# Performance work log

Measured on AMD Instinct MI355X. Metric: run time of the kernel, lower is better.

Reference implementation:

```python
import jax, jax.numpy as jnp
import numpy as np

DIM = 1024
NUM_HEADS = 16
HEAD_DIM = DIM // NUM_HEADS
SCALE = HEAD_DIM ** -0.5


def setup_inputs() -> dict:
    key = jax.random.key(0)
    ks = jax.random.split(key, 6)
    B, N, C = 2, 2048, DIM
    std = C ** -0.5
    return {
        "x_t": jax.random.normal(ks[0], (B, N, C), dtype=jnp.float32),
        "x_s": jax.random.normal(ks[1], (B, N, C), dtype=jnp.float32),
        "W_q": jax.random.normal(ks[2], (C, C), dtype=jnp.float32) * std,
        "W_kv": jax.random.normal(ks[3], (C, 2 * C), dtype=jnp.float32) * std,
        "W_fuse": jax.random.normal(ks[4], (C, C), dtype=jnp.float32) * std,
        "b_fuse": jax.random.normal(ks[5], (C,), dtype=jnp.float32) * 0.01,
    }


def reference(x_t, x_s, W_q, W_kv, W_fuse, b_fuse):
    B, N, C = x_t.shape
    H, D = NUM_HEADS, HEAD_DIM
    # q projection (no bias, qkv_bias=False): [B,N,C] -> [B,H,N,D]
    q = (x_t @ W_q).reshape(B, N, H, D).transpose(0, 2, 1, 3)
    # kv projection: [B,N,2C] -> k,v each [B,H,N,D]
    kv = (x_s @ W_kv).reshape(B, N, 2, H, D).transpose(2, 0, 3, 1, 4)
    k, v = kv[0], kv[1]
    # attention scores [B,H,N,N]
    attn = jnp.einsum("bhnd,bhmd->bhnm", q, k) * SCALE
    attn = jax.nn.softmax(attn, axis=-1)
    # weighted values -> [B,N,C]
    a = jnp.einsum("bhnm,bhmd->bhnd", attn, v).transpose(0, 2, 1, 3).reshape(B, N, C)
    # fuse projection (with bias); dropouts are identity (p=0)
    return a @ W_fuse + b_fuse
```

## Files before the change

### kernel.cpp

```cpp
#include <hip/hip_runtime.h>

#define SEQ 2048

typedef short short8 __attribute__((ext_vector_type(8)));
typedef float floatx4 __attribute__((ext_vector_type(4)));
typedef unsigned int uint2v __attribute__((ext_vector_type(2)));
typedef unsigned int uint4v __attribute__((ext_vector_type(4)));
typedef __fp16 f16x8 __attribute__((ext_vector_type(8)));

static __device__ __forceinline__ unsigned short f2bf(float f) {
    unsigned int u = __builtin_bit_cast(unsigned int, f);
    u = (u + 0x7fffu + ((u >> 16) & 1u)) >> 16;
    return (unsigned short)u;
}

#if __has_builtin(__builtin_amdgcn_cvt_pk_bf16_f32)
typedef __bf16 bf16x2 __attribute__((ext_vector_type(2)));
static __device__ __forceinline__ unsigned int pk_bf16(float a, float b) {
    bf16x2 v = __builtin_amdgcn_cvt_pk_bf16_f32(a, b);
    return __builtin_bit_cast(unsigned int, v);
}
#else
static __device__ __forceinline__ unsigned int pk_bf16(float a, float b) {
    return (unsigned int)f2bf(a) | ((unsigned int)f2bf(b) << 16);
}
#endif

static __device__ __forceinline__ unsigned int pk_f16(float a, float b) {
    auto v = __builtin_amdgcn_cvt_pkrtz(a, b);
    return __builtin_bit_cast(unsigned int, v);
}

#define GLD16(gp, lp)                                                        \
    __builtin_amdgcn_global_load_lds(                                        \
        (const __attribute__((address_space(1))) unsigned int*)(gp),         \
        (__attribute__((address_space(3))) unsigned int*)(lp), 16, 0, 0)

__global__ void cvt2_kernel(const float4* __restrict__ a, const float4* __restrict__ b,
                            ushort4* __restrict__ oa, ushort4* __restrict__ ob, float sa) {
    int i = blockIdx.x * blockDim.x + threadIdx.x;
    if (i < 1048576) {
        float4 v = a[i];
        ushort4 o;
        o.x = f2bf(v.x * sa); o.y = f2bf(v.y * sa);
        o.z = f2bf(v.z * sa); o.w = f2bf(v.w * sa);
        oa[i] = o;
    } else {
        int j = i - 1048576;
        float4 v = b[j];
        ushort4 o;
        o.x = f2bf(v.x); o.y = f2bf(v.y);
        o.z = f2bf(v.z); o.w = f2bf(v.w);
        ob[j] = o;
    }
}

__global__ void transpose_all(const float* __restrict__ Wq, const float* __restrict__ Wkv,
                              const float* __restrict__ Wf,
                              unsigned short* __restrict__ oq, unsigned short* __restrict__ okv,
                              unsigned short* __restrict__ of_) {
    __shared__ float tile[32][33];
    int bx = blockIdx.x;
    const float* in; unsigned short* out; int N, t;
    if (bx < 1024)      { in = Wq;  out = oq;  N = 1024; t = bx; }
    else if (bx < 3072) { in = Wkv; out = okv; N = 2048; t = bx - 1024; }
    else                { in = Wf;  out = of_; N = 1024; t = bx - 3072; }
    int nb = N >> 5;
    int n0 = (t % nb) * 32, k0 = (t / nb) * 32;
    int tx = threadIdx.x, ty = threadIdx.y;
#pragma unroll
    for (int i = 0; i < 4; i++)
        tile[ty + i * 8][tx] = in[(size_t)(k0 + ty + i * 8) * N + n0 + tx];
    __syncthreads();
#pragma unroll
    for (int i = 0; i < 4; i++)
        out[(size_t)(n0 + ty + i * 8) * 1024 + k0 + tx] = f2bf(tile[tx][ty + i * 8]);
}

__global__ __launch_bounds__(256, 3)
void gemm_qkv(const unsigned short* __restrict__ xt,
              const unsigned short* __restrict__ xs,
              const unsigned short* __restrict__ wq,
              const unsigned short* __restrict__ wkv,
              unsigned short* __restrict__ q_ws,
              unsigned short* __restrict__ k_ws,
              unsigned short* __restrict__ vt_ws) {
    __shared__ unsigned short sA[128][64];
    __shared__ unsigned short sB[128][64];
    int tid = threadIdx.x, wave = tid >> 6, lane = tid & 63;
    int l15 = lane & 15, quad = lane >> 4;
    int cx = blockIdx.x;
    bool isq = cx < 8;
    const unsigned short* A  = isq ? xt : xs;
    const unsigned short* Bt = isq ? wq : wkv;
    int C0 = (isq ? cx : cx - 8) * 128;
    int R0 = blockIdx.y * 128;
    int wr = (wave >> 1) * 64, wc = (wave & 1) * 64;
    int srow = lane >> 3, scol = (lane & 7) * 8;

    floatx4 acc[4][4];
#pragma unroll
    for (int i = 0; i < 4; i++)
#pragma unroll
        for (int j = 0; j < 4; j++) acc[i][j] = (floatx4){0.f, 0.f, 0.f, 0.f};

    for (int kt = 0; kt < 16; kt++) {
        __syncthreads();
#pragma unroll
        for (int c = 0; c < 4; c++) {
            int rb = wave * 32 + c * 8;
            GLD16(&A [(size_t)(R0 + rb + srow) * 1024 + kt * 64 + scol], &sA[rb][0]);
            GLD16(&Bt[(size_t)(C0 + rb + srow) * 1024 + kt * 64 + scol], &sB[rb][0]);
        }
        __syncthreads();
#pragma unroll
        for (int ks = 0; ks < 2; ks++) {
            short8 af[4], bf[4];
#pragma unroll
            for (int mt = 0; mt < 4; mt++)
                af[mt] = *(const short8*)&sA[wr + mt * 16 + l15][ks * 32 + quad * 8];
#pragma unroll
            for (int nt = 0; nt < 4; nt++)
                bf[nt] = *(const short8*)&sB[wc + nt * 16 + l15][ks * 32 + quad * 8];
#pragma unroll
            for (int mt = 0; mt < 4; mt++)
#pragma unroll
                for (int nt = 0; nt < 4; nt++)
                    acc[mt][nt] = __builtin_amdgcn_mfma_f32_16x16x32_bf16(af[mt], bf[nt], acc[mt][nt], 0, 0, 0);
        }
    }

    int b = R0 >> 11, nb0 = (R0 & 2047) + wr;
#pragma unroll
    for (int mt = 0; mt < 4; mt++) {
#pragma unroll
        for (int nt = 0; nt < 4; nt++) {
            int col = C0 + wc + nt * 16 + l15;
            if (isq) {
                int h = col >> 6, d = col & 63;
#pragma unroll
                for (int r = 0; r < 4; r++) {
                    int n = nb0 + mt * 16 + quad * 4 + r;
                    q_ws[((size_t)((b * 16 + h) * 2048 + n)) * 64 + d] = f2bf(acc[mt][nt][r]);
                }
            } else if (col < 1024) {
                int h = col >> 6, d = col & 63;
#pragma unroll
                for (int r = 0; r < 4; r++) {
                    int n = nb0 + mt * 16 + quad * 4 + r;
                    k_ws[((size_t)((b * 16 + h) * 2048 + n)) * 64 + (d ^ ((n & 7) << 3))] = f2bf(acc[mt][nt][r]);
                }
            } else {
                int cc = col - 1024, h = cc >> 6, d = cc & 63;
                int n0 = nb0 + mt * 16 + quad * 4;
                int coln = (n0 & ~63) | ((n0 & 63) ^ ((d & 7) << 3));
                uint2v pk;
                pk.x = pk_f16(acc[mt][nt][0], acc[mt][nt][1]);
                pk.y = pk_f16(acc[mt][nt][2], acc[mt][nt][3]);
                *(uint2v*)&vt_ws[((size_t)((b * 16 + h) * 64 + d)) * 2048 + coln] = pk;
            }
        }
    }
}

__global__ __launch_bounds__(256, 3)
void gemm_fuse(const unsigned short* __restrict__ A,
               const unsigned short* __restrict__ Bt,
               float* __restrict__ out, const float* __restrict__ bias) {
    __shared__ unsigned short sA[128][64];
    __shared__ unsigned short sB[64][64];
    int tid = threadIdx.x, wave = tid >> 6, lane = tid & 63;
    int l15 = lane & 15, quad = lane >> 4;
    int R0 = blockIdx.y * 128, C0 = blockIdx.x * 64;
    int wr = (wave >> 1) * 64, wc = (wave & 1) * 32;
    int srow = lane >> 3, scol = (lane & 7) * 8;

    floatx4 acc[4][2];
#pragma unroll
    for (int i = 0; i < 4; i++)
#pragma unroll
        for (int j = 0; j < 2; j++) acc[i][j] = (floatx4){0.f, 0.f, 0.f, 0.f};

    for (int kt = 0; kt < 16; kt++) {
        __syncthreads();
#pragma unroll
        for (int c = 0; c < 4; c++) {
            int rb = wave * 32 + c * 8;
            GLD16(&A[(size_t)(R0 + rb + srow) * 1024 + kt * 64 + scol], &sA[rb][0]);
        }
#pragma unroll
        for (int c = 0; c < 2; c++) {
            int rb = wave * 16 + c * 8;
            GLD16(&Bt[(size_t)(C0 + rb + srow) * 1024 + kt * 64 + scol], &sB[rb][0]);
        }
        __syncthreads();
#pragma unroll
        for (int ks = 0; ks < 2; ks++) {
            short8 af[4], bf[2];
#pragma unroll
            for (int mt = 0; mt < 4; mt++)
                af[mt] = *(const short8*)&sA[wr + mt * 16 + l15][ks * 32 + quad * 8];
#pragma unroll
            for (int nt = 0; nt < 2; nt++)
                bf[nt] = *(const short8*)&sB[wc + nt * 16 + l15][ks * 32 + quad * 8];
#pragma unroll
            for (int mt = 0; mt < 4; mt++)
#pragma unroll
                for (int nt = 0; nt < 2; nt++)
                    acc[mt][nt] = __builtin_amdgcn_mfma_f32_16x16x32_bf16(af[mt], bf[nt], acc[mt][nt], 0, 0, 0);
        }
    }

#pragma unroll
    for (int mt = 0; mt < 4; mt++) {
#pragma unroll
        for (int r = 0; r < 4; r++) {
            int row = R0 + wr + mt * 16 + quad * 4 + r;
#pragma unroll
            for (int nt = 0; nt < 2; nt++) {
                int col = C0 + wc + nt * 16 + l15;
                out[(size_t)row * 1024 + col] = acc[mt][nt][r] + bias[col];
            }
        }
    }
}

__global__ __launch_bounds__(256, 2)
void attn_kernel(const unsigned short* __restrict__ Q,
                 const unsigned short* __restrict__ K,
                 const unsigned short* __restrict__ Vt,
                 unsigned short* __restrict__ Aout) {
    __shared__ __align__(16) unsigned short smem[32768];
    __shared__ float lred[4][4][16];

    int tid = threadIdx.x, wave = tid >> 6, lane = tid & 63;
    int l15 = lane & 15, quad = lane >> 4;

    int id = blockIdx.x;
    int logical = (id & 7) * 128 + (id >> 3);
    int bh = logical >> 5, qt = logical & 31;
    int b = bh >> 4, h = bh & 15;
    int qr0 = qt * 64;

    const unsigned short* Qp = Q + (size_t)bh * SEQ * 64;
    const unsigned short* Kp = K + (size_t)bh * SEQ * 64;
    const unsigned short* Vp = Vt + (size_t)bh * 64 * SEQ;

    int srow = lane >> 3, scol = (lane & 7) * 8;
    int wk0 = wave * 16;

#define STAGE(tile, kb)                                                       \
    {                                                                         \
        _Pragma("unroll")                                                     \
        for (int j = 0; j < 2; j++) {                                         \
            int rb = wk0 + j * 8;                                             \
            GLD16(&Kp[(size_t)((tile) * 64 + rb + srow) * 64 + scol],         \
                  &smem[(kb) + rb * 64]);                                     \
            GLD16(&Vp[(size_t)(rb + srow) * 2048 + (tile) * 64 + scol],       \
                  &smem[16384 + (kb) + rb * 64]);                             \
        }                                                                     \
    }

    short8 qf[4][2];
#pragma unroll
    for (int nt = 0; nt < 4; nt++)
#pragma unroll
        for (int ks = 0; ks < 2; ks++)
            qf[nt][ks] = *(const short8*)&Qp[(size_t)(qr0 + nt * 16 + l15) * 64 + ks * 32 + quad * 8];

    STAGE(0, 0) STAGE(1, 4096) STAGE(2, 8192) STAGE(3, 12288)

    floatx4 of[4][4];
#pragma unroll
    for (int i = 0; i < 4; i++)
#pragma unroll
        for (int j = 0; j < 4; j++) of[i][j] = (floatx4){0.f, 0.f, 0.f, 0.f};
    floatx4 of_l[4];
#pragma unroll
    for (int i = 0; i < 4; i++) of_l[i] = (floatx4){0.f, 0.f, 0.f, 0.f};

    f16x8 vones;
#pragma unroll
    for (int i = 0; i < 8; i++) vones[i] = (__fp16)1.0f;

    int krow = wk0 + l15;
    int ksw = (l15 & 7) << 3;
    int kaddr0 = krow * 64 + ((quad * 8) ^ ksw);
    int kaddr1 = krow * 64 + ((32 + quad * 8) ^ ksw);
    int vcol = (wk0 + quad * 4) ^ ksw;

    asm volatile("s_waitcnt vmcnt(0)" ::: "memory");
    __syncthreads();

    auto compute_pair = [&](int kb) {
        __builtin_amdgcn_s_setprio(1);
        uint2v pka[4], pkb[4];
        {
            short8 kf0 = *(const short8*)&smem[kb + kaddr0];
            short8 kf1 = *(const short8*)&smem[kb + kaddr1];
#pragma unroll
            for (int nt = 0; nt < 4; nt++) {
                floatx4 z = (floatx4){0.f, 0.f, 0.f, 0.f};
                floatx4 s = __builtin_amdgcn_mfma_f32_16x16x32_bf16(kf0, qf[nt][0], z, 0, 0, 0);
                s = __builtin_amdgcn_mfma_f32_16x16x32_bf16(kf1, qf[nt][1], s, 0, 0, 0);
                pka[nt].x = pk_f16(__builtin_amdgcn_exp2f(s[0]), __builtin_amdgcn_exp2f(s[1]));
                pka[nt].y = pk_f16(__builtin_amdgcn_exp2f(s[2]), __builtin_amdgcn_exp2f(s[3]));
            }
        }
        {
            short8 kf0 = *(const short8*)&smem[kb + 4096 + kaddr0];
            short8 kf1 = *(const short8*)&smem[kb + 4096 + kaddr1];
#pragma unroll
            for (int nt = 0; nt < 4; nt++) {
                floatx4 z = (floatx4){0.f, 0.f, 0.f, 0.f};
                floatx4 s = __builtin_amdgcn_mfma_f32_16x16x32_bf16(kf0, qf[nt][0], z, 0, 0, 0);
                s = __builtin_amdgcn_mfma_f32_16x16x32_bf16(kf1, qf[nt][1], s, 0, 0, 0);
                pkb[nt].x = pk_f16(__builtin_amdgcn_exp2f(s[0]), __builtin_amdgcn_exp2f(s[1]));
                pkb[nt].y = pk_f16(__builtin_amdgcn_exp2f(s[2]), __builtin_amdgcn_exp2f(s[3]));
            }
        }
#pragma unroll
        for (int dt = 0; dt < 4; dt++) {
            int vbase = 16384 + kb + (dt * 16 + l15) * 64 + vcol;
            uint2v va = *(const uint2v*)&smem[vbase];
            uint2v vb = *(const uint2v*)&smem[vbase + 4096];
            f16x8 vf = __builtin_bit_cast(f16x8, (uint4v){va.x, va.y, vb.x, vb.y});
#pragma unroll
            for (int nt = 0; nt < 4; nt++) {
                f16x8 pf = __builtin_bit_cast(f16x8, (uint4v){pka[nt].x, pka[nt].y, pkb[nt].x, pkb[nt].y});
                of[dt][nt] = __builtin_amdgcn_mfma_f32_16x16x32_f16(vf, pf, of[dt][nt], 0, 0, 0);
            }
        }
#pragma unroll
        for (int nt = 0; nt < 4; nt++) {
            f16x8 pf = __builtin_bit_cast(f16x8, (uint4v){pka[nt].x, pka[nt].y, pkb[nt].x, pkb[nt].y});
            of_l[nt] = __builtin_amdgcn_mfma_f32_16x16x32_f16(vones, pf, of_l[nt], 0, 0, 0);
        }
        __builtin_amdgcn_s_setprio(0);
    };

#pragma unroll 2
    for (int p = 0; p < 14; p++) {
        int kb = (p & 1) * 8192;
        compute_pair(kb);
        __builtin_amdgcn_sched_barrier(0);
        asm volatile("s_barrier" ::: "memory");
        STAGE(2 * p + 4, kb)
        STAGE(2 * p + 5, kb + 4096)
        asm volatile("s_waitcnt vmcnt(8)" ::: "memory");
        asm volatile("s_barrier" ::: "memory");
        __builtin_amdgcn_sched_barrier(0);
    }
    compute_pair(0);
    asm volatile("s_waitcnt vmcnt(0)" ::: "memory");
    asm volatile("s_barrier" ::: "memory");
    compute_pair(8192);
#undef STAGE

    if (quad == 0) {
#pragma unroll
        for (int nt = 0; nt < 4; nt++) lred[wave][nt][l15] = of_l[nt][0];
    }
    __syncthreads();

    float* red = (float*)smem;

#define RED_WRITE(C, DTC)                                                          \
    _Pragma("unroll")                                                              \
    for (int nt = 0; nt < 4; nt++)                                                 \
        *(floatx4*)&red[((C) * 4 + wave) * 1024 + nt * 256 + lane * 4] = of[DTC][nt];

#define RED_STORE(DT, C, W0, W1, W2)                                               \
    {                                                                              \
        size_t obase = (size_t)(b * SEQ + qr0) * 1024 + h * 64 + (DT) * 16 + quad * 4; \
        _Pragma("unroll")                                                          \
        for (int nt = 0; nt < 4; nt++) {                                           \
            floatx4 a0 = *(const floatx4*)&red[((C) * 4 + (W0)) * 1024 + nt * 256 + lane * 4]; \
            floatx4 a1 = *(const floatx4*)&red[((C) * 4 + (W1)) * 1024 + nt * 256 + lane * 4]; \
            floatx4 a2 = *(const floatx4*)&red[((C) * 4 + (W2)) * 1024 + nt * 256 + lane * 4]; \
            floatx4 s = of[DT][nt] + a0 + a1 + a2;                                 \
            float lt = lred[0][nt][l15] + lred[1][nt][l15] + lred[2][nt][l15] + lred[3][nt][l15]; \
            float inv = 1.f / lt;                                                  \
            uint2v o;                                                              \
            o.x = pk_bf16(s[0] * inv, s[1] * inv);                                 \
            o.y = pk_bf16(s[2] * inv, s[3] * inv);                                 \
            *(uint2v*)&Aout[obase + (size_t)(nt * 16 + l15) * 1024] = o;           \
        }                                                                          \
    }

    RED_WRITE(0, 0)
    RED_WRITE(1, 1)
    __syncthreads();
    if (wave == 0)      RED_STORE(0, 0, 1, 2, 3)
    else if (wave == 1) RED_STORE(1, 1, 0, 2, 3)
    __syncthreads();
    RED_WRITE(0, 2)
    RED_WRITE(1, 3)
    __syncthreads();
    if (wave == 2)      RED_STORE(2, 0, 0, 1, 3)
    else if (wave == 3) RED_STORE(3, 1, 0, 1, 2)
#undef RED_WRITE
#undef RED_STORE
}

extern "C" void kernel_launch(void* const* d_in, const int* in_sizes, int n_in,
                              void* d_out, int out_size, void* d_ws, size_t ws_size,
                              hipStream_t stream) {
    const float* x_t  = (const float*)d_in[0];
    const float* x_s  = (const float*)d_in[1];
    const float* W_q  = (const float*)d_in[2];
    const float* W_kv = (const float*)d_in[3];
    const float* W_f  = (const float*)d_in[4];
    const float* b_f  = (const float*)d_in[5];
    float* out = (float*)d_out;

    char* ws = (char*)d_ws;
    const size_t MB = 1u << 20;
    unsigned short* xt_bf = (unsigned short*)(ws);
    unsigned short* xs_bf = (unsigned short*)(ws + 8 * MB);
    unsigned short* wq_t  = (unsigned short*)(ws + 16 * MB);
    unsigned short* wkv_t = (unsigned short*)(ws + 18 * MB);
    unsigned short* wf_t  = (unsigned short*)(ws + 22 * MB);
    unsigned short* q_ws  = (unsigned short*)(ws + 24 * MB);
    unsigned short* k_ws  = (unsigned short*)(ws + 32 * MB);
    unsigned short* vt_ws = (unsigned short*)(ws + 40 * MB);
    unsigned short* a_ws  = (unsigned short*)(ws + 48 * MB);

    cvt2_kernel<<<8192, 256, 0, stream>>>((const float4*)x_t, (const float4*)x_s,
                                          (ushort4*)xt_bf, (ushort4*)xs_bf,
                                          0.125f * 1.44269504088896340736f);
    transpose_all<<<4096, dim3(32, 8), 0, stream>>>(W_q, W_kv, W_f, wq_t, wkv_t, wf_t);

    gemm_qkv<<<dim3(24, 32), 256, 0, stream>>>(xt_bf, xs_bf, wq_t, wkv_t, q_ws, k_ws, vt_ws);
    attn_kernel<<<1024, 256, 0, stream>>>(q_ws, k_ws, vt_ws, a_ws);
    gemm_fuse<<<dim3(16, 32), 256, 0, stream>>>(a_ws, wf_t, out, b_f);
}
```

Baseline: 201.4 us.

## Give each wave private K/V smem slices and drop block barriers in attention loop

Each wave now stages only its own 16-key slice of K and V into a private region of shared memory, so the main loop no longer needs the two s_barrier calls per iteration. V^T is written unswizzled by the projection kernel, and the swizzle moves into the load addressing and the LDS read pattern. This removes cross-wave synchronisation stalls and lets waves drift independently. The risks are more LDS bank conflicts from the new layout, smaller per-wave global loads, and a dependence on per-wave vmcnt ordering for correctness.

```diff
diff --git a/kernel.cpp b/kernel.cpp
--- a/kernel.cpp
+++ b/kernel.cpp
@@ -152,12 +152,11 @@
                 }
             } else {
                 int cc = col - 1024, h = cc >> 6, d = cc & 63;
-                int n0 = nb0 + mt * 16 + quad * 4;
-                int coln = (n0 & ~63) | ((n0 & 63) ^ ((d & 7) << 3));
+                int n = nb0 + mt * 16 + quad * 4;
                 uint2v pk;
                 pk.x = pk_f16(acc[mt][nt][0], acc[mt][nt][1]);
                 pk.y = pk_f16(acc[mt][nt][2], acc[mt][nt][3]);
-                *(uint2v*)&vt_ws[((size_t)((b * 16 + h) * 64 + d)) * 2048 + coln] = pk;
+                *(uint2v*)&vt_ws[((size_t)((b * 16 + h) * 64 + d)) * 2048 + n] = pk;
             }
         }
     }
@@ -246,18 +245,22 @@
     const unsigned short* Kp = K + (size_t)bh * SEQ * 64;
     const unsigned short* Vp = Vt + (size_t)bh * 64 * SEQ;
 
-    int srow = lane >> 3, scol = (lane & 7) * 8;
     int wk0 = wave * 16;
-
-#define STAGE(tile, kb)                                                       \
+    int WB = wave * 8192;
+
+#define STAGE(t, s)                                                           \
     {                                                                         \
         _Pragma("unroll")                                                     \
+        for (int j = 0; j < 2; j++)                                           \
+            GLD16(&Kp[(size_t)((t) * 64 + wk0 + j * 8 + (lane >> 3)) * 64 +   \
+                      (lane & 7) * 8],                                        \
+                  &smem[WB + (s) * 2048 + j * 512]);                          \
+        _Pragma("unroll")                                                     \
         for (int j = 0; j < 2; j++) {                                         \
-            int rb = wk0 + j * 8;                                             \
-            GLD16(&Kp[(size_t)((tile) * 64 + rb + srow) * 64 + scol],         \
-                  &smem[(kb) + rb * 64]);                                     \
-            GLD16(&Vp[(size_t)(rb + srow) * 2048 + (tile) * 64 + scol],       \
-                  &smem[16384 + (kb) + rb * 64]);                             \
+            int dsrc = j * 32 + (lane >> 1);                                  \
+            int hb = (((lane & 1) ^ ((dsrc >> 2) & 1)) << 3);                 \
+            GLD16(&Vp[(size_t)dsrc * 2048 + (t) * 64 + wk0 + hb],             \
+                  &smem[WB + (s) * 2048 + 1024 + j * 512]);                   \
         }                                                                     \
     }
 
@@ -268,7 +271,7 @@
         for (int ks = 0; ks < 2; ks++)
             qf[nt][ks] = *(const short8*)&Qp[(size_t)(qr0 + nt * 16 + l15) * 64 + ks * 32 + quad * 8];
 
-    STAGE(0, 0) STAGE(1, 4096) STAGE(2, 8192) STAGE(3, 12288)
+    STAGE(0, 0) STAGE(1, 1) STAGE(2, 2) STAGE(3, 3)
 
     floatx4 of[4][4];
 #pragma unroll
@@ -283,21 +286,19 @@
 #pragma unroll
     for (int i = 0; i < 8; i++) vones[i] = (__fp16)1.0f;
 
-    int krow = wk0 + l15;
     int ksw = (l15 & 7) << 3;
-    int kaddr0 = krow * 64 + ((quad * 8) ^ ksw);
-    int kaddr1 = krow * 64 + ((32 + quad * 8) ^ ksw);
-    int vcol = (wk0 + quad * 4) ^ ksw;
+    int ka0 = l15 * 64 + ((quad * 8) ^ ksw);
+    int ka1 = l15 * 64 + ((32 + quad * 8) ^ ksw);
 
     asm volatile("s_waitcnt vmcnt(0)" ::: "memory");
-    __syncthreads();
-
-    auto compute_pair = [&](int kb) {
+
+    auto compute_pair = [&](int sA, int sB) {
+        int b0 = WB + sA * 2048, b1 = WB + sB * 2048;
         __builtin_amdgcn_s_setprio(1);
         uint2v pka[4], pkb[4];
         {
-            short8 kf0 = *(const short8*)&smem[kb + kaddr0];
-            short8 kf1 = *(const short8*)&smem[kb + kaddr1];
+            short8 kf0 = *(const short8*)&smem[b0 + ka0];
+            short8 kf1 = *(const short8*)&smem[b0 + ka1];
 #pragma unroll
             for (int nt = 0; nt < 4; nt++) {
                 floatx4 z = (floatx4){0.f, 0.f, 0.f, 0.f};
@@ -308,8 +309,8 @@
             }
         }
         {
-            short8 kf0 = *(const short8*)&smem[kb + 4096 + kaddr0];
-            short8 kf1 = *(const short8*)&smem[kb + 4096 + kaddr1];
+            short8 kf0 = *(const short8*)&smem[b1 + ka0];
+            short8 kf1 = *(const short8*)&smem[b1 + ka1];
 #pragma unroll
             for (int nt = 0; nt < 4; nt++) {
                 floatx4 z = (floatx4){0.f, 0.f, 0.f, 0.f};
@@ -321,19 +322,22 @@
         }
 #pragma unroll
         for (int dt = 0; dt < 4; dt++) {
-            int vbase = 16384 + kb + (dt * 16 + l15) * 64 + vcol;
-            uint2v va = *(const uint2v*)&smem[vbase];
-            uint2v vb = *(const uint2v*)&smem[vbase + 4096];
+            int d = dt * 16 + l15;
+            int vo = d * 16 + ((quad * 4) ^ (((d >> 2) & 1) << 3));
+            uint2v va = *(const uint2v*)&smem[b0 + 1024 + vo];
+            uint2v vb = *(const uint2v*)&smem[b1 + 1024 + vo];
             f16x8 vf = __builtin_bit_cast(f16x8, (uint4v){va.x, va.y, vb.x, vb.y});
 #pragma unroll
             for (int nt = 0; nt < 4; nt++) {
-                f16x8 pf = __builtin_bit_cast(f16x8, (uint4v){pka[nt].x, pka[nt].y, pkb[nt].x, pkb[nt].y});
+                f16x8 pf = __builtin_bit_cast(f16x8,
+                    (uint4v){pka[nt].x, pka[nt].y, pkb[nt].x, pkb[nt].y});
                 of[dt][nt] = __builtin_amdgcn_mfma_f32_16x16x32_f16(vf, pf, of[dt][nt], 0, 0, 0);
             }
         }
 #pragma unroll
         for (int nt = 0; nt < 4; nt++) {
-            f16x8 pf = __builtin_bit_cast(f16x8, (uint4v){pka[nt].x, pka[nt].y, pkb[nt].x, pkb[nt].y});
+            f16x8 pf = __builtin_bit_cast(f16x8,
+                (uint4v){pka[nt].x, pka[nt].y, pkb[nt].x, pkb[nt].y});
             of_l[nt] = __builtin_amdgcn_mfma_f32_16x16x32_f16(vones, pf, of_l[nt], 0, 0, 0);
         }
         __builtin_amdgcn_s_setprio(0);
@@ -341,20 +345,14 @@
 
 #pragma unroll 2
     for (int p = 0; p < 14; p++) {
-        int kb = (p & 1) * 8192;
-        compute_pair(kb);
-        __builtin_amdgcn_sched_barrier(0);
-        asm volatile("s_barrier" ::: "memory");
-        STAGE(2 * p + 4, kb)
-        STAGE(2 * p + 5, kb + 4096)
+        int sA = (p & 1) * 2;
+        compute_pair(sA, sA + 1);
+        STAGE(2 * p + 4, sA) STAGE(2 * p + 5, sA + 1)
         asm volatile("s_waitcnt vmcnt(8)" ::: "memory");
-        asm volatile("s_barrier" ::: "memory");
-        __builtin_amdgcn_sched_barrier(0);
-    }
-    compute_pair(0);
+    }
+    compute_pair(0, 1);
     asm volatile("s_waitcnt vmcnt(0)" ::: "memory");
-    asm volatile("s_barrier" ::: "memory");
-    compute_pair(8192);
+    compute_pair(2, 3);
 #undef STAGE
 
     if (quad == 0) {
```

Measured after the change: 205.3 us. About the same (+2.0%).
